# Kernel tuning notes

Measured on AMD Instinct MI355X. Metric: run time of the kernel, lower is better.

Reference implementation:

```python
import jax, jax.numpy as jnp
import numpy as np

B, T, F, H = 256, 32, 128, 128
NUM_FILTERS, KH, KW, NUM_CLASSES = 64, 2, 2, 2
FLAT = NUM_FILTERS * (T - KH + 1) * (2 * F - KW + 1)  # 64*31*255 = 505920


def setup_inputs() -> dict:
    key = jax.random.key(0)
    ks = jax.random.split(key, 12)
    inp = {
        "X_nume": jax.random.normal(ks[0], (B, T, F), jnp.float32),
        "att_W": jax.random.uniform(ks[1], (F, H), jnp.float32),
        "att_U": jax.random.uniform(ks[2], (F, H), jnp.float32),
        "att_V": jax.random.uniform(ks[3], (H, 1), jnp.float32),
        "conv_w": jax.random.normal(ks[4], (NUM_FILTERS, 1, KH, KW), jnp.float32) * 0.5,
        "conv_b": jax.random.normal(ks[5], (NUM_FILTERS,), jnp.float32) * 0.1,
        "w1": jax.random.normal(ks[6], (FLAT, 256), jnp.float32) * (1.0 / np.sqrt(FLAT)),
        "b1": jnp.zeros((256,), jnp.float32),
        "w2": jax.random.normal(ks[7], (256, 32), jnp.float32) * (1.0 / np.sqrt(256)),
        "b2": jnp.zeros((32,), jnp.float32),
        "w3": jax.random.normal(ks[8], (32, NUM_CLASSES), jnp.float32) * (1.0 / np.sqrt(32)),
        "b3": jnp.zeros((NUM_CLASSES,), jnp.float32),
    }
    return inp


def reference(X_nume, att_W, att_U, att_V, conv_w, conv_b, w1, b1, w2, b2, w3, b3):
    X = X_nume  # [B, T, F]
    # --- additive attention, fully batched (replaces O(T^2) python loops) ---
    xw = jnp.einsum("btf,fh->bth", X, att_W)  # query proj [B,T,H]
    xu = jnp.einsum("btf,fh->bth", X, att_U)  # key proj   [B,T,H]
    # e[b,i,j] = V^T tanh(x_i W + x_j U)
    scores = jnp.squeeze(jnp.tanh(xw[:, :, None, :] + xu[:, None, :, :]) @ att_V, -1)  # [B,T,T]
    alpha = jax.nn.softmax(scores, axis=-1)  # softmax over j (includes diagonal)
    # context excludes j == i (original skips j == index AFTER softmax)
    mask = 1.0 - jnp.eye(T, dtype=X.dtype)
    c = jnp.einsum("bij,bjf->bif", alpha * mask, X)  # [B,T,F]
    feat = jnp.concatenate([X, c], axis=-1)  # [B,T,2F]
    # --- conv ---
    conv_in = feat[:, None, :, :]  # [B,1,T,2F]
    conv = jax.lax.conv_general_dilated(
        conv_in, conv_w, window_strides=(1, 1), padding="VALID",
        dimension_numbers=("NCHW", "OIHW", "NCHW"))
    conv = jax.nn.relu(conv + conv_b[None, :, None, None])  # [B,64,T-1,2F-1]
    # --- MLP head ---
    flat = conv.reshape(conv.shape[0], -1)
    h = jax.nn.relu(flat @ w1 + b1)
    h = jax.nn.relu(h @ w2 + b2)
    return h @ w3 + b3
```

## Files before the change

### kernel.cpp

```cpp
#include <hip/hip_runtime.h>
#include <hip/hip_bf16.h>

#define B_ 256
#define T_ 32
#define F_ 128
#define H_ 128
#define NF 64
#define OH 31
#define OW 255
#define POS_TOTAL (OH*OW)
#define N1 256
#define KT 248

typedef __attribute__((ext_vector_type(8))) short bf16x8;
typedef __attribute__((ext_vector_type(4))) float f32x4;

__device__ __forceinline__ unsigned int cvtpk(float lo, float hi) {
    unsigned int r;
    asm("v_cvt_pk_bf16_f32 %0, %1, %2" : "=v"(r) : "v"(lo), "v"(hi));
    return r;
}

__device__ __forceinline__ void gll16(const void* g, void* l) {
    __builtin_amdgcn_global_load_lds(
        (const __attribute__((address_space(1))) void*)g,
        (__attribute__((address_space(3))) void*)l, 16, 0, 0);
}

__global__ __launch_bounds__(256) void k_attn(
    const float* __restrict__ X, const float* __restrict__ W,
    const float* __restrict__ U, const float* __restrict__ V,
    float* __restrict__ featL)
{
    __shared__ float Xs[T_][F_];
    __shared__ float xw[T_][H_];
    __shared__ float xu[T_][H_];
    __shared__ float sc[T_][T_];
    __shared__ float Vs[H_];

    const int b = blockIdx.x;
    const int t = threadIdx.x;
    const float* Xb = X + (size_t)b * T_ * F_;

    for (int idx = t; idx < T_*F_; idx += 256) ((float*)Xs)[idx] = Xb[idx];
    if (t < H_) Vs[t] = V[t];
    __syncthreads();

    {
        const int h = t & 127, half = t >> 7;
        float aw[16], au[16];
        #pragma unroll
        for (int r = 0; r < 16; r++) { aw[r] = 0.f; au[r] = 0.f; }
        for (int f = 0; f < F_; f++) {
            const float wv = W[f*H_ + h];
            const float uv = U[f*H_ + h];
            #pragma unroll
            for (int r = 0; r < 16; r++) {
                const float xv = Xs[half*16 + r][f];
                aw[r] += xv * wv;
                au[r] += xv * uv;
            }
        }
        #pragma unroll
        for (int r = 0; r < 16; r++) {
            xw[half*16 + r][h] = aw[r];
            xu[half*16 + r][h] = au[r];
        }
    }
    __syncthreads();

    {
        const int i = t >> 3;
        const int j0 = (t & 7) * 4;
        float s0 = 0.f, s1 = 0.f, s2 = 0.f, s3 = 0.f;
        for (int h = 0; h < H_; h++) {
            const float xwv = xw[i][h];
            const float vv  = Vs[h];
            s0 += tanhf(xwv + xu[j0+0][h]) * vv;
            s1 += tanhf(xwv + xu[j0+1][h]) * vv;
            s2 += tanhf(xwv + xu[j0+2][h]) * vv;
            s3 += tanhf(xwv + xu[j0+3][h]) * vv;
        }
        sc[i][j0+0] = s0; sc[i][j0+1] = s1; sc[i][j0+2] = s2; sc[i][j0+3] = s3;
    }
    __syncthreads();

    if (t < T_) {
        float m = -1e30f;
        #pragma unroll
        for (int j = 0; j < T_; j++) m = fmaxf(m, sc[t][j]);
        float sum = 0.f;
        #pragma unroll
        for (int j = 0; j < T_; j++) sum += expf(sc[t][j] - m);
        const float inv = 1.f / sum;
        #pragma unroll
        for (int j = 0; j < T_; j++) {
            const float a = expf(sc[t][j] - m) * inv;
            sc[t][j] = (j == t) ? 0.f : a;
        }
    }
    __syncthreads();

    for (int idx = t; idx < T_*F_; idx += 256) {
        const int row = idx >> 7, f = idx & 127;
        float acc = 0.f;
        #pragma unroll
        for (int j = 0; j < T_; j++) acc += sc[row][j] * Xs[j][f];
        float* fr = featL + (size_t)b*8192 + row*256;
        fr[f]       = Xs[row][f];
        fr[128 + f] = acc;
    }
}

__global__ __launch_bounds__(256) void k_tr(
    const float* __restrict__ src, float* __restrict__ dst)
{
    __shared__ float tile[32][33];
    const int rc0 = blockIdx.x * 32;
    const int b0  = blockIdx.y * 32;
    const int tx = threadIdx.x & 31;
    const int ty = threadIdx.x >> 5;
    #pragma unroll
    for (int r = 0; r < 32; r += 8)
        tile[ty + r][tx] = src[(size_t)(b0 + ty + r)*8192 + rc0 + tx];
    __syncthreads();
    #pragma unroll
    for (int r = 0; r < 32; r += 8)
        dst[(size_t)(rc0 + ty + r)*256 + b0 + tx] = tile[tx][ty + r];
}

__global__ __launch_bounds__(512, 2) void k_gemm1(
    const float* __restrict__ featT, const float* __restrict__ cw,
    const float* __restrict__ cb, const float* __restrict__ w1,
    float* __restrict__ partial)
{
    __shared__ float          WsL[3][16][260];
    __shared__ unsigned short As[2][256][40];
    __shared__ float cwL[256];
    __shared__ float cbL[64];

    const int t  = threadIdx.x;
    const int nt = blockIdx.x;
    const int kt = blockIdx.y;
    const int nb = nt * 128;
    const int pos0 = kt * 32;

    if (t < 256) cwL[t] = cw[t];
    if (t < 64)  cbL[t] = cb[t];

    const int rm = t & 255;
    const int ph = t >> 8;
    const int pbase = pos0 + ph*16;

    const int lane = t & 63, wid = t >> 6;
    const int wm = (wid & 3) * 64;
    const int wn = (wid >> 2) * 64;
    const int fr = lane & 15, fq = lane >> 4;

    f32x4 acc[4][4];
    #pragma unroll
    for (int i = 0; i < 4; i++)
        #pragma unroll
        for (int j = 0; j < 4; j++)
            acc[i][j] = (f32x4){0.f, 0.f, 0.f, 0.f};

    float p0[16], p1[16], p2[16], p3[16];
    #pragma unroll
    for (int i = 0; i < 16; i++) {
        int p = pbase + i; if (p > POS_TOTAL-1) p = POS_TOTAL-1;
        const int y = p / 255, x = p - y*255;
        const float* fp = featT + ((size_t)(y*256 + x))*256 + rm;
        p0[i] = fp[0];
        p1[i] = fp[256];
        p2[i] = fp[65536];
        p3[i] = fp[65536 + 256];
    }

#define GLLW(F2)                                                               \
    {                                                                          \
        const int wb_ = (F2) % 3;                                              \
        _Pragma("unroll")                                                      \
        for (int j = 0; j < 2; j++) {                                          \
            const int pr_ = wid*2 + j;                         \
            int pos_ = pos0 + pr_*2 + (lane >> 5);                             \
            if (pos_ > POS_TOTAL-1) pos_ = POS_TOTAL-1;                        \
            gll16(w1 + ((size_t)(F2)*POS_TOTAL + pos_)*N1 + nb                 \
                     + ((lane & 31) << 2),                                     \
                  &WsL[wb_][pr_][0]);                                          \
        }                                                                      \
    }

#define CONVW(F2)                                                              \
    {                                                                          \
        const float4 cc_ = *(const float4*)&cwL[(F2)*4];                       \
        const float cbv_ = cbL[F2];                                            \
        unsigned int pk_[8];                                                   \
        _Pragma("unroll")                                                      \
        for (int i2 = 0; i2 < 8; i2++) {                                       \
            float v0_ = p0[2*i2]*cc_.x + p1[2*i2]*cc_.y                        \
                      + p2[2*i2]*cc_.z + p3[2*i2]*cc_.w + cbv_;                \
            float v1_ = p0[2*i2+1]*cc_.x + p1[2*i2+1]*cc_.y                    \
                      + p2[2*i2+1]*cc_.z + p3[2*i2+1]*cc_.w + cbv_;            \
            v0_ = (pbase + 2*i2     < POS_TOTAL) ? fmaxf(v0_, 0.f) : 0.f;      \
            v1_ = (pbase + 2*i2 + 1 < POS_TOTAL) ? fmaxf(v1_, 0.f) : 0.f;      \
            pk_[i2] = cvtpk(v0_, v1_);                                         \
        }                                                                      \
        *(uint4*)&As[(F2) & 1][rm][ph*16    ] = *(uint4*)&pk_[0];              \
        *(uint4*)&As[(F2) & 1][rm][ph*16 + 8] = *(uint4*)&pk_[4];              \
    }

    GLLW(0);
    GLLW(1);
    __syncthreads();
    CONVW(0);
    CONVW(1);
    asm volatile("s_waitcnt lgkmcnt(0)" ::: "memory");
    __builtin_amdgcn_s_barrier();

    #pragma unroll 1
    for (int f = 0; f < 64; f++) {
        const int cur = f & 1;
        const int wb  = f % 3;

        bf16x8 af_[4];
        #pragma unroll
        for (int mg = 0; mg < 4; mg++)
            af_[mg] = *(const bf16x8*)&As[cur][wm + mg*16 + fr][fq*8];
        asm volatile("s_waitcnt lgkmcnt(0)" ::: "memory");
        __builtin_amdgcn_s_barrier();

        if (f < 62) {
            GLLW(f + 2);
            CONVW(f + 2);
        }

        {
            __builtin_amdgcn_s_setprio(1);
            #pragma unroll
            for (int ng = 0; ng < 4; ng++) {
                const int colb = wn + ng*16 + fr;
                float w_[8];
                #pragma unroll
                for (int j = 0; j < 8; j++)
                    w_[j] = WsL[wb][fq*4 + (j >> 1)][(j & 1)*128 + colb];
                bf16x8 bfr;
                unsigned int* bu = (unsigned int*)&bfr;
                #pragma unroll
                for (int j2 = 0; j2 < 4; j2++)
                    bu[j2] = cvtpk(w_[2*j2], w_[2*j2+1]);
                #pragma unroll
                for (int mg = 0; mg < 4; mg++)
                    acc[mg][ng] = __builtin_amdgcn_mfma_f32_16x16x32_bf16(
                        af_[mg], bfr, acc[mg][ng], 0, 0, 0);
            }
            __builtin_amdgcn_s_setprio(0);
        }

        if (f < 62) {
            asm volatile("s_waitcnt vmcnt(2) lgkmcnt(0)" ::: "memory");
        } else {
            asm volatile("s_waitcnt vmcnt(0) lgkmcnt(0)" ::: "memory");
        }
        __builtin_amdgcn_s_barrier();
    }

    float* pp = partial + (size_t)kt * (256*N1) + nb;
    #pragma unroll
    for (int mg = 0; mg < 4; mg++)
        #pragma unroll
        for (int ng = 0; ng < 4; ng++) {
            const int col = wn + ng*16 + fr;
            #pragma unroll
            for (int j = 0; j < 4; j++) {
                const int row = wm + mg*16 + fq*4 + j;
                pp[(size_t)row*N1 + col] = acc[mg][ng][j];
            }
        }
#undef GLLW
#undef CONVW
}

__global__ __launch_bounds__(256) void k_head(
    const float* __restrict__ partial,
    const float* __restrict__ b1, const float* __restrict__ w2,
    const float* __restrict__ b2, const float* __restrict__ w3,
    const float* __restrict__ b3, float* __restrict__ out)
{
    __shared__ float h1s[256];
    __shared__ float h2s[32];
    const int b = blockIdx.x, t = threadIdx.x;

    const float* pb = partial + (size_t)b*N1 + t;
    float s0 = 0.f, s1 = 0.f, s2 = 0.f, s3 = 0.f;
    #pragma unroll 2
    for (int kt = 0; kt < KT; kt += 4) {
        s0 += pb[(size_t)(kt+0)*65536];
        s1 += pb[(size_t)(kt+1)*65536];
        s2 += pb[(size_t)(kt+2)*65536];
        s3 += pb[(size_t)(kt+3)*65536];
    }
    h1s[t] = fmaxf(b1[t] + ((s0+s1)+(s2+s3)), 0.f);
    __syncthreads();

    if (t < 32) {
        float s2v = b2[t];
        for (int i = 0; i < 256; i++) s2v += h1s[i] * w2[i*32 + t];
        h2s[t] = fmaxf(s2v, 0.f);
    }
    __syncthreads();

    if (t < 2) {
        float s3v = b3[t];
        #pragma unroll
        for (int i = 0; i < 32; i++) s3v += h2s[i] * w3[i*2 + t];
        out[b*2 + t] = s3v;
    }
}

extern "C" void kernel_launch(void* const* d_in, const int* in_sizes, int n_in,
                              void* d_out, int out_size, void* d_ws, size_t ws_size,
                              hipStream_t stream) {
    const float* X    = (const float*)d_in[0];
    const float* attW = (const float*)d_in[1];
    const float* attU = (const float*)d_in[2];
    const float* attV = (const float*)d_in[3];
    const float* cw   = (const float*)d_in[4];
    const float* cb   = (const float*)d_in[5];
    const float* w1   = (const float*)d_in[6];
    const float* b1   = (const float*)d_in[7];
    const float* w2   = (const float*)d_in[8];
    const float* b2   = (const float*)d_in[9];
    const float* w3   = (const float*)d_in[10];
    const float* b3   = (const float*)d_in[11];
    float* out = (float*)d_out;

    float* featL   = (float*)d_ws;
    float* featT   = (float*)((char*)d_ws + (8u<<20));
    float* partial = (float*)((char*)d_ws + (16u<<20));

    k_attn <<<dim3(B_),       dim3(256), 0, stream>>>(X, attW, attU, attV, featL);
    k_tr   <<<dim3(256, 8),   dim3(256), 0, stream>>>(featL, featT);
    k_gemm1<<<dim3(2, KT),    dim3(512), 0, stream>>>(featT, cw, cb, w1, partial);
    k_head <<<dim3(B_),       dim3(256), 0, stream>>>(partial, b1, w2, b2, w3, b3, out);
}
```

Baseline: 309.7 us.

## Restructure conv+GEMM1 into full-N row tiles with bf16 swizzled LDS weights

Each GEMM1 block now covers all 256 output columns for one conv-output row segment (y, 32 x positions), so the grid drops from 2xKT to KT and the conv activations are computed once instead of twice. The 2x2 conv window is loaded as 17 top and 17 bottom values with horizontal reuse, not four independent loads per position. w1 is loaded through registers, converted to bf16 once, and stored in XOR-swizzled LDS, replacing async global-to-LDS fp32 loads that were converted inside the MFMA loop. The K-step doubles to two filters per iteration. Each wave now holds 8x4 accumulators, which raises register pressure and may lower occupancy.

```diff
diff --git a/kernel.cpp b/kernel.cpp
--- a/kernel.cpp
+++ b/kernel.cpp
@@ -19,12 +19,6 @@
     unsigned int r;
     asm("v_cvt_pk_bf16_f32 %0, %1, %2" : "=v"(r) : "v"(lo), "v"(hi));
     return r;
-}
-
-__device__ __forceinline__ void gll16(const void* g, void* l) {
-    __builtin_amdgcn_global_load_lds(
-        (const __attribute__((address_space(1))) void*)g,
-        (__attribute__((address_space(3))) void*)l, 16, 0, 0);
 }
 
 __global__ __launch_bounds__(256) void k_attn(
@@ -134,139 +128,134 @@
     const float* __restrict__ cb, const float* __restrict__ w1,
     float* __restrict__ partial)
 {
-    __shared__ float          WsL[3][16][260];
-    __shared__ unsigned short As[2][256][40];
+    __shared__ unsigned short As[2][256*64];
+    __shared__ unsigned short Ws[2][256*64];
     __shared__ float cwL[256];
     __shared__ float cbL[64];
 
     const int t  = threadIdx.x;
-    const int nt = blockIdx.x;
-    const int kt = blockIdx.y;
-    const int nb = nt * 128;
-    const int pos0 = kt * 32;
+    const int kt = blockIdx.x;
+    const int y  = kt >> 3;
+    const int x0 = (kt & 7) * 32;
 
     if (t < 256) cwL[t] = cw[t];
     if (t < 64)  cbL[t] = cb[t];
 
     const int rm = t & 255;
     const int ph = t >> 8;
-    const int pbase = pos0 + ph*16;
-
+    const int r0 = (t & 15) * 4;
+    const int c0 = (t >> 4) * 8;
     const int lane = t & 63, wid = t >> 6;
-    const int wm = (wid & 3) * 64;
-    const int wn = (wid >> 2) * 64;
+    const int wm = (wid >> 2) * 128;
+    const int wn = (wid & 3) * 64;
     const int fr = lane & 15, fq = lane >> 4;
 
-    f32x4 acc[4][4];
-    #pragma unroll
-    for (int i = 0; i < 4; i++)
+    f32x4 acc[8][4];
+    #pragma unroll
+    for (int i = 0; i < 8; i++)
         #pragma unroll
         for (int j = 0; j < 4; j++)
             acc[i][j] = (f32x4){0.f, 0.f, 0.f, 0.f};
 
-    float p0[16], p1[16], p2[16], p3[16];
-    #pragma unroll
-    for (int i = 0; i < 16; i++) {
-        int p = pbase + i; if (p > POS_TOTAL-1) p = POS_TOTAL-1;
-        const int y = p / 255, x = p - y*255;
-        const float* fp = featT + ((size_t)(y*256 + x))*256 + rm;
-        p0[i] = fp[0];
-        p1[i] = fp[256];
-        p2[i] = fp[65536];
-        p3[i] = fp[65536 + 256];
-    }
-
-#define GLLW(F2)                                                               \
+    float topv[17], botv[17];
+    #pragma unroll
+    for (int i = 0; i < 17; i++) {
+        int xc = x0 + ph*16 + i; if (xc > 255) xc = 255;
+        topv[i] = featT[((size_t)(y*256 + xc))*256 + rm];
+        botv[i] = featT[((size_t)((y+1)*256 + xc))*256 + rm];
+    }
+
+    float wvf[4][8];
+
+#define W_LOADS(S)                                                             \
     {                                                                          \
-        const int wb_ = (F2) % 3;                                              \
+        const int fl_ = r0 >> 5;                                               \
+        const int f_  = 2*(S) + fl_;                                           \
         _Pragma("unroll")                                                      \
-        for (int j = 0; j < 2; j++) {                                          \
-            const int pr_ = wid*2 + j;                         \
-            int pos_ = pos0 + pr_*2 + (lane >> 5);                             \
-            if (pos_ > POS_TOTAL-1) pos_ = POS_TOTAL-1;                        \
-            gll16(w1 + ((size_t)(F2)*POS_TOTAL + pos_)*N1 + nb                 \
-                     + ((lane & 31) << 2),                                     \
-                  &WsL[wb_][pr_][0]);                                          \
+        for (int jj = 0; jj < 4; jj++) {                                       \
+            int xc_ = x0 + (r0 & 31) + jj; if (xc_ > 254) xc_ = 254;           \
+            const float* wp_ = w1 + ((size_t)(f_*POS_TOTAL + y*255 + xc_))*N1  \
+                                  + c0;                                        \
+            *(float4*)&wvf[jj][0] = *(const float4*)&wp_[0];                   \
+            *(float4*)&wvf[jj][4] = *(const float4*)&wp_[4];                   \
         }                                                                      \
     }
 
-#define CONVW(F2)                                                              \
+#define STAGE(BUF, S)                                                          \
     {                                                                          \
-        const float4 cc_ = *(const float4*)&cwL[(F2)*4];                       \
-        const float cbv_ = cbL[F2];                                            \
-        unsigned int pk_[8];                                                   \
         _Pragma("unroll")                                                      \
-        for (int i2 = 0; i2 < 8; i2++) {                                       \
-            float v0_ = p0[2*i2]*cc_.x + p1[2*i2]*cc_.y                        \
-                      + p2[2*i2]*cc_.z + p3[2*i2]*cc_.w + cbv_;                \
-            float v1_ = p0[2*i2+1]*cc_.x + p1[2*i2+1]*cc_.y                    \
-                      + p2[2*i2+1]*cc_.z + p3[2*i2+1]*cc_.w + cbv_;            \
-            v0_ = (pbase + 2*i2     < POS_TOTAL) ? fmaxf(v0_, 0.f) : 0.f;      \
-            v1_ = (pbase + 2*i2 + 1 < POS_TOTAL) ? fmaxf(v1_, 0.f) : 0.f;      \
-            pk_[i2] = cvtpk(v0_, v1_);                                         \
+        for (int i = 0; i < 8; i++) {                                          \
+            const int n_ = c0 + i;                                             \
+            uint2 v_;                                                          \
+            v_.x = cvtpk(wvf[0][i], wvf[1][i]);                                \
+            v_.y = cvtpk(wvf[2][i], wvf[3][i]);                                \
+            const int blk_ = (r0 >> 3) ^ (n_ & 7);                             \
+            *(uint2*)&Ws[BUF][n_*64 + blk_*8 + (r0 & 7)] = v_;                 \
         }                                                                      \
-        *(uint4*)&As[(F2) & 1][rm][ph*16    ] = *(uint4*)&pk_[0];              \
-        *(uint4*)&As[(F2) & 1][rm][ph*16 + 8] = *(uint4*)&pk_[4];              \
-    }
-
-    GLLW(0);
-    GLLW(1);
-    __syncthreads();
-    CONVW(0);
-    CONVW(1);
+        _Pragma("unroll")                                                      \
+        for (int fl = 0; fl < 2; fl++) {                                       \
+            const int f_ = 2*(S) + fl;                                         \
+            const float4 cc_ = *(const float4*)&cwL[f_*4];                     \
+            const float cbv_ = cbL[f_];                                        \
+            unsigned int pk_[4];                                               \
+            _Pragma("unroll")                                                  \
+            for (int i2 = 0; i2 < 8; i2++) {                                   \
+                const int i0 = 2*i2, i1 = 2*i2 + 1;                            \
+                float v0_ = topv[i0]*cc_.x + topv[i0+1]*cc_.y                  \
+                          + botv[i0]*cc_.z + botv[i0+1]*cc_.w + cbv_;          \
+                float v1_ = topv[i1]*cc_.x + topv[i1+1]*cc_.y                  \
+                          + botv[i1]*cc_.z + botv[i1+1]*cc_.w + cbv_;          \
+                v0_ = (x0 + ph*16 + i0 < 255) ? fmaxf(v0_, 0.f) : 0.f;         \
+                v1_ = (x0 + ph*16 + i1 < 255) ? fmaxf(v1_, 0.f) : 0.f;         \
+                pk_[i2 & 3] = cvtpk(v0_, v1_);                                 \
+                if ((i2 & 3) == 3) {                                           \
+                    const int kb_ = fl*4 + ph*2 + (i2 >> 2);                   \
+                    *(uint4*)&As[BUF][rm*64 + ((kb_ ^ (rm & 7))*8)]            \
+                        = *(uint4*)&pk_[0];                                    \
+                }                                                              \
+            }                                                                  \
+        }                                                                      \
+    }
+
+    W_LOADS(0);
+    __syncthreads();
+    STAGE(0, 0);
     asm volatile("s_waitcnt lgkmcnt(0)" ::: "memory");
     __builtin_amdgcn_s_barrier();
 
     #pragma unroll 1
-    for (int f = 0; f < 64; f++) {
-        const int cur = f & 1;
-        const int wb  = f % 3;
-
-        bf16x8 af_[4];
-        #pragma unroll
-        for (int mg = 0; mg < 4; mg++)
-            af_[mg] = *(const bf16x8*)&As[cur][wm + mg*16 + fr][fq*8];
+    for (int s = 0; s < 32; s++) {
+        const int cur = s & 1;
+        if (s < 31) W_LOADS(s + 1);
+
+        __builtin_amdgcn_s_setprio(1);
+        #pragma unroll
+        for (int kc = 0; kc < 2; kc++) {
+            const int sw = ((kc*4 + fq) ^ (fr & 7)) * 8;
+            bf16x8 bf_[4];
+            #pragma unroll
+            for (int ng = 0; ng < 4; ng++)
+                bf_[ng] = *(const bf16x8*)&Ws[cur][(wn + ng*16 + fr)*64 + sw];
+            #pragma unroll
+            for (int mg = 0; mg < 8; mg++) {
+                const bf16x8 af_ =
+                    *(const bf16x8*)&As[cur][(wm + mg*16 + fr)*64 + sw];
+                #pragma unroll
+                for (int ng = 0; ng < 4; ng++)
+                    acc[mg][ng] = __builtin_amdgcn_mfma_f32_16x16x32_bf16(
+                        af_, bf_[ng], acc[mg][ng], 0, 0, 0);
+            }
+        }
+        __builtin_amdgcn_s_setprio(0);
+
+        if (s < 31) STAGE(cur ^ 1, s + 1);
         asm volatile("s_waitcnt lgkmcnt(0)" ::: "memory");
         __builtin_amdgcn_s_barrier();
-
-        if (f < 62) {
-            GLLW(f + 2);
-            CONVW(f + 2);
-        }
-
-        {
-            __builtin_amdgcn_s_setprio(1);
-            #pragma unroll
-            for (int ng = 0; ng < 4; ng++) {
-                const int colb = wn + ng*16 + fr;
-                float w_[8];
-                #pragma unroll
-                for (int j = 0; j < 8; j++)
-                    w_[j] = WsL[wb][fq*4 + (j >> 1)][(j & 1)*128 + colb];
-                bf16x8 bfr;
-                unsigned int* bu = (unsigned int*)&bfr;
-                #pragma unroll
-                for (int j2 = 0; j2 < 4; j2++)
-                    bu[j2] = cvtpk(w_[2*j2], w_[2*j2+1]);
-                #pragma unroll
-                for (int mg = 0; mg < 4; mg++)
-                    acc[mg][ng] = __builtin_amdgcn_mfma_f32_16x16x32_bf16(
-                        af_[mg], bfr, acc[mg][ng], 0, 0, 0);
-            }
-            __builtin_amdgcn_s_setprio(0);
-        }
-
-        if (f < 62) {
-            asm volatile("s_waitcnt vmcnt(2) lgkmcnt(0)" ::: "memory");
-        } else {
-            asm volatile("s_waitcnt vmcnt(0) lgkmcnt(0)" ::: "memory");
-        }
-        __builtin_amdgcn_s_barrier();
-    }
-
-    float* pp = partial + (size_t)kt * (256*N1) + nb;
-    #pragma unroll
-    for (int mg = 0; mg < 4; mg++)
+    }
+
+    float* pp = partial + (size_t)kt * (256*N1);
+    #pragma unroll
+    for (int mg = 0; mg < 8; mg++)
         #pragma unroll
         for (int ng = 0; ng < 4; ng++) {
             const int col = wn + ng*16 + fr;
@@ -276,8 +265,8 @@
                 pp[(size_t)row*N1 + col] = acc[mg][ng][j];
             }
         }
-#undef GLLW
-#undef CONVW
+#undef W_LOADS
+#undef STAGE
 }
 
 __global__ __launch_bounds__(256) void k_head(
@@ -340,6 +329,6 @@
 
     k_attn <<<dim3(B_),       dim3(256), 0, stream>>>(X, attW, attU, attV, featL);
     k_tr   <<<dim3(256, 8),   dim3(256), 0, stream>>>(featL, featT);
-    k_gemm1<<<dim3(2, KT),    dim3(512), 0, stream>>>(featT, cw, cb, w1, partial);
+    k_gemm1<<<dim3(KT),       dim3(512), 0, stream>>>(featT, cw, cb, w1, partial);
     k_head <<<dim3(B_),       dim3(256), 0, stream>>>(partial, b1, w2, b2, w3, b3, out);
 }
```

After: 269.5 us. -13.0%, faster.
